# Kernel optimization log

Measured on AMD Instinct MI355X. Metric: run time of the kernel, lower is better.

The kernel has to match this reference:

```python
import jax, jax.numpy as jnp
import numpy as np

B, T = 16, 16384
K, D, H = 512, 64, 64
COMMIT = 0.25
LN_EPS = 1e-5


def setup_inputs() -> dict:
    key = jax.random.key(0)
    ks = jax.random.split(key, 4)
    t = jax.random.randint(ks[0], (B, T, 1), 0, K, dtype=jnp.int32)
    W1 = jax.random.normal(ks[1], (1, H), dtype=jnp.float32) * 0.5
    b1 = jnp.zeros((H,), dtype=jnp.float32)
    ln_g = jnp.ones((H,), dtype=jnp.float32)
    ln_b = jnp.zeros((H,), dtype=jnp.float32)
    W2 = jax.random.normal(ks[2], (H, D), dtype=jnp.float32) * (1.0 / np.sqrt(H))
    b2 = jnp.zeros((D,), dtype=jnp.float32)
    # torch init: uniform(-1/K, 1/K)
    codebook = jax.random.uniform(ks[3], (K, D), dtype=jnp.float32,
                                  minval=-1.0 / K, maxval=1.0 / K)
    return {"t": t, "W1": W1, "b1": b1, "ln_g": ln_g, "ln_b": ln_b,
            "W2": W2, "b2": b2, "codebook": codebook}


def _encoder(t, W1, b1, ln_g, ln_b, W2, b2):
    norm_t = t.astype(jnp.float32) / (K - 1) * 2.0 - 1.0  # [B,T,1]
    h = norm_t @ W1 + b1                                   # [B,T,H]
    mu = jnp.mean(h, axis=-1, keepdims=True)
    var = jnp.mean(jnp.square(h - mu), axis=-1, keepdims=True)
    h = (h - mu) * jax.lax.rsqrt(var + LN_EPS) * ln_g + ln_b
    h = jax.nn.relu(h)
    return h @ W2 + b2                                     # [B,T,D]


def reference(t, W1, b1, ln_g, ln_b, W2, b2, codebook):
    z = _encoder(t, W1, b1, ln_g, ln_b, W2, b2)            # [B,T,D]
    flat_z = z.reshape(-1, D)                               # [N,D]
    # squared distances: ||z||^2 - 2 z.e^T + ||e||^2  -> [N,K]
    dist = (jnp.sum(flat_z * flat_z, axis=1, keepdims=True)
            - 2.0 * flat_z @ codebook.T
            + jnp.sum(codebook * codebook, axis=1))
    idx = jnp.argmin(dist, axis=1)                          # [N]
    quantized = codebook[idx]                               # [N,D]
    sg = jax.lax.stop_gradient
    loss = (jnp.mean(jnp.square(quantized - sg(flat_z)))
            + COMMIT * jnp.mean(jnp.square(sg(quantized) - flat_z)))
    q = flat_z + sg(quantized - flat_z)                     # straight-through
    return q.reshape(z.shape), idx.reshape(z.shape[0], -1), loss
```

## Files before the change

### kernel.cpp

```cpp
#include <hip/hip_runtime.h>

#define Kc 512
#define Dc 64
#define Hc 64
#define Bc 16
#define Tc 16384
#define Nt (Bc * Tc)
#define LN_EPS 1e-5f
#define LOSS_SCALE (1.25f / 16777216.0f)

#define GATHER_BLOCKS 4096
#define GATHER_THREADS 256
#define GATHER_ITERS 4

__global__ __launch_bounds__(256) void precompute_kernel(
    const float* __restrict__ W1, const float* __restrict__ b1,
    const float* __restrict__ ln_g, const float* __restrict__ ln_b,
    const float* __restrict__ W2, const float* __restrict__ b2,
    const float* __restrict__ cb,
    float* __restrict__ q_table, float* __restrict__ idxf_table,
    float* __restrict__ d2_table)
{
    const int v   = blockIdx.x;
    const int tid = threadIdx.x;

    __shared__ float s_h[Hc];
    __shared__ float s_z[Dc];
    __shared__ float s_bd[4];
    __shared__ int   s_bk[4];
    __shared__ int   s_win;
    __shared__ float s_wd;

    if (tid < 64) {
        const int lane = tid;
        const float norm_t = (float)v * (2.0f / (float)(Kc - 1)) - 1.0f;
        float h = norm_t * W1[lane] + b1[lane];

        float s = h;
        #pragma unroll
        for (int o = 32; o > 0; o >>= 1) s += __shfl_xor(s, o);
        const float mu = s * (1.0f / (float)Hc);
        const float d = h - mu;
        float vs = d * d;
        #pragma unroll
        for (int o = 32; o > 0; o >>= 1) vs += __shfl_xor(vs, o);
        const float var = vs * (1.0f / (float)Hc);
        float hn = d * rsqrtf(var + LN_EPS) * ln_g[lane] + ln_b[lane];
        hn = fmaxf(hn, 0.0f);
        s_h[lane] = hn;
        __builtin_amdgcn_s_waitcnt(0);
        float z = b2[lane];
        #pragma unroll
        for (int hh = 0; hh < Hc; ++hh) z = fmaf(s_h[hh], W2[hh * Dc + lane], z);
        s_z[lane] = z;
    }
    __syncthreads();

    const float4* z4 = (const float4*)s_z;
    float best_d = 3.4e38f;
    int best_k = 0;
    #pragma unroll
    for (int half = 0; half < 2; ++half) {
        const int k = tid + half * 256;
        const float4* e4 = (const float4*)(cb + k * Dc);
        float dist = 0.0f;
        #pragma unroll
        for (int q = 0; q < 16; ++q) {
            const float4 e = e4[q];
            const float4 zz = z4[q];
            float d0 = zz.x - e.x, d1 = zz.y - e.y, d2 = zz.z - e.z, d3 = zz.w - e.w;
            dist = fmaf(d0, d0, dist); dist = fmaf(d1, d1, dist);
            dist = fmaf(d2, d2, dist); dist = fmaf(d3, d3, dist);
        }
        if (dist < best_d) { best_d = dist; best_k = k; }
    }
    #pragma unroll
    for (int o = 32; o > 0; o >>= 1) {
        const float od = __shfl_xor(best_d, o);
        const int   ok = __shfl_xor(best_k, o);
        if (od < best_d || (od == best_d && ok < best_k)) { best_d = od; best_k = ok; }
    }
    if ((tid & 63) == 0) { s_bd[tid >> 6] = best_d; s_bk[tid >> 6] = best_k; }
    __syncthreads();
    if (tid == 0) {
        float bd = s_bd[0]; int bk = s_bk[0];
        #pragma unroll
        for (int w = 1; w < 4; ++w) {
            const float od = s_bd[w]; const int ok = s_bk[w];
            if (od < bd || (od == bd && ok < bk)) { bd = od; bk = ok; }
        }
        s_win = bk; s_wd = bd;
    }
    __syncthreads();

    if (tid < 64) q_table[v * Dc + tid] = cb[s_win * Dc + tid];
    if (tid == 0) { idxf_table[v] = (float)s_win; d2_table[v] = s_wd; }
}

__global__ __launch_bounds__(GATHER_THREADS) void gather_kernel(
    const int* __restrict__ t, const float* __restrict__ q_table,
    const float* __restrict__ idxf_table, const float* __restrict__ d2_table,
    float* __restrict__ out_q, float* __restrict__ out_idx,
    float* __restrict__ partials)
{
    const int tid = threadIdx.x;
    const int g0  = blockIdx.x * GATHER_THREADS + tid;
    const int stride = GATHER_BLOCKS * GATHER_THREADS;

    float lsum = 0.0f;
    #pragma unroll
    for (int i = 0; i < GATHER_ITERS; ++i) {
        const int g     = g0 + i * stride;
        const int token = g >> 4;
        const int part  = g & 15;
        const int tv = t[token];
        const float4 q = ((const float4*)q_table)[(tv << 4) + part];
        ((float4*)out_q)[g] = q;
        if (part == 0) {
            out_idx[token] = idxf_table[tv];
            lsum += d2_table[tv];
        }
    }

    #pragma unroll
    for (int o = 32; o > 0; o >>= 1) lsum += __shfl_xor(lsum, o);
    __shared__ float s_partial[4];
    if ((tid & 63) == 0) s_partial[tid >> 6] = lsum;
    __syncthreads();
    if (tid == 0)
        partials[blockIdx.x] =
            s_partial[0] + s_partial[1] + s_partial[2] + s_partial[3];
}

__global__ __launch_bounds__(256) void loss_reduce_kernel(
    const float* __restrict__ partials, float* __restrict__ out_loss)
{
    const int tid = threadIdx.x;
    float s = 0.0f;
    #pragma unroll
    for (int i = 0; i < GATHER_BLOCKS / 256; ++i)
        s += partials[i * 256 + tid];
    #pragma unroll
    for (int o = 32; o > 0; o >>= 1) s += __shfl_xor(s, o);
    __shared__ float s_partial[4];
    if ((tid & 63) == 0) s_partial[tid >> 6] = s;
    __syncthreads();
    if (tid == 0)
        out_loss[0] = (s_partial[0] + s_partial[1] + s_partial[2] + s_partial[3])
                      * LOSS_SCALE;
}

extern "C" void kernel_launch(void* const* d_in, const int* in_sizes, int n_in,
                              void* d_out, int out_size, void* d_ws, size_t ws_size,
                              hipStream_t stream) {
    const int*   t        = (const int*)d_in[0];
    const float* W1       = (const float*)d_in[1];
    const float* b1       = (const float*)d_in[2];
    const float* ln_g     = (const float*)d_in[3];
    const float* ln_b     = (const float*)d_in[4];
    const float* W2       = (const float*)d_in[5];
    const float* b2       = (const float*)d_in[6];
    const float* codebook = (const float*)d_in[7];

    float* out      = (float*)d_out;
    float* out_q    = out;
    float* out_idx  = out + (size_t)Nt * Dc;
    float* out_loss = out_idx + Nt;

    float* ws        = (float*)d_ws;
    float* q_table   = ws;
    float* idxf_tab  = ws + Kc * Dc;
    float* d2_tab    = idxf_tab + Kc;
    float* partials  = d2_tab + Kc;

    precompute_kernel<<<Kc, 256, 0, stream>>>(
        W1, b1, ln_g, ln_b, W2, b2, codebook,
        q_table, idxf_tab, d2_tab);

    gather_kernel<<<GATHER_BLOCKS, GATHER_THREADS, 0, stream>>>(
        t, q_table, idxf_tab, d2_tab, out_q, out_idx, partials);

    loss_reduce_kernel<<<1, 256, 0, stream>>>(partials, out_loss);
}
```

Before: 110.8 us.

## Fuse loss reduction into gather via last-block atomic counter, nontemporal stores

Removes the separate loss-reduce kernel launch: each gather block publishes its partial sum with a release store and bumps an atomic counter, and the last block to finish does the final reduction. Output stores of the quantized tensor become nontemporal so the large streaming write bypasses cache retention. The gather grid shrinks to 1024 blocks with 16 iterations each, which cuts the number of partials. The cost is one atomic per block and a dependence on the counter being reset in the precompute kernel.

```diff
diff --git a/kernel.cpp b/kernel.cpp
--- a/kernel.cpp
+++ b/kernel.cpp
@@ -9,9 +9,11 @@
 #define LN_EPS 1e-5f
 #define LOSS_SCALE (1.25f / 16777216.0f)
 
-#define GATHER_BLOCKS 4096
+#define GATHER_BLOCKS 1024
 #define GATHER_THREADS 256
-#define GATHER_ITERS 4
+#define GATHER_ITERS 16
+
+typedef float v4f __attribute__((ext_vector_type(4)));
 
 __global__ __launch_bounds__(256) void precompute_kernel(
     const float* __restrict__ W1, const float* __restrict__ b1,
@@ -19,10 +21,12 @@
     const float* __restrict__ W2, const float* __restrict__ b2,
     const float* __restrict__ cb,
     float* __restrict__ q_table, float* __restrict__ idxf_table,
-    float* __restrict__ d2_table)
+    float* __restrict__ d2_table, int* __restrict__ counter)
 {
     const int v   = blockIdx.x;
     const int tid = threadIdx.x;
+
+    if (v == 0 && tid == 0) *counter = 0;
 
     __shared__ float s_h[Hc];
     __shared__ float s_z[Dc];
@@ -101,7 +105,8 @@
     const int* __restrict__ t, const float* __restrict__ q_table,
     const float* __restrict__ idxf_table, const float* __restrict__ d2_table,
     float* __restrict__ out_q, float* __restrict__ out_idx,
-    float* __restrict__ partials)
+    float* __restrict__ partials, int* __restrict__ counter,
+    float* __restrict__ out_loss)
 {
     const int tid = threadIdx.x;
     const int g0  = blockIdx.x * GATHER_THREADS + tid;
@@ -115,7 +120,8 @@
         const int part  = g & 15;
         const int tv = t[token];
         const float4 q = ((const float4*)q_table)[(tv << 4) + part];
-        ((float4*)out_q)[g] = q;
+        const v4f qv = { q.x, q.y, q.z, q.w };
+        __builtin_nontemporal_store(qv, &((v4f*)out_q)[g]);
         if (part == 0) {
             out_idx[token] = idxf_table[tv];
             lsum += d2_table[tv];
@@ -125,29 +131,34 @@
     #pragma unroll
     for (int o = 32; o > 0; o >>= 1) lsum += __shfl_xor(lsum, o);
     __shared__ float s_partial[4];
+    __shared__ int   s_done;
     if ((tid & 63) == 0) s_partial[tid >> 6] = lsum;
     __syncthreads();
-    if (tid == 0)
-        partials[blockIdx.x] =
+    if (tid == 0) {
+        const float bs =
             s_partial[0] + s_partial[1] + s_partial[2] + s_partial[3];
-}
+        __hip_atomic_store(&partials[blockIdx.x], bs, __ATOMIC_RELEASE,
+                           __HIP_MEMORY_SCOPE_AGENT);
+        const int prev = __hip_atomic_fetch_add(counter, 1, __ATOMIC_ACQ_REL,
+                                                __HIP_MEMORY_SCOPE_AGENT);
+        s_done = (prev == GATHER_BLOCKS - 1) ? 1 : 0;
+    }
+    __syncthreads();
 
-__global__ __launch_bounds__(256) void loss_reduce_kernel(
-    const float* __restrict__ partials, float* __restrict__ out_loss)
-{
-    const int tid = threadIdx.x;
-    float s = 0.0f;
-    #pragma unroll
-    for (int i = 0; i < GATHER_BLOCKS / 256; ++i)
-        s += partials[i * 256 + tid];
-    #pragma unroll
-    for (int o = 32; o > 0; o >>= 1) s += __shfl_xor(s, o);
-    __shared__ float s_partial[4];
-    if ((tid & 63) == 0) s_partial[tid >> 6] = s;
-    __syncthreads();
-    if (tid == 0)
-        out_loss[0] = (s_partial[0] + s_partial[1] + s_partial[2] + s_partial[3])
-                      * LOSS_SCALE;
+    if (s_done) {
+        float s = 0.0f;
+        #pragma unroll
+        for (int i = 0; i < GATHER_BLOCKS / GATHER_THREADS; ++i)
+            s += __hip_atomic_load(&partials[i * GATHER_THREADS + tid],
+                                   __ATOMIC_ACQUIRE, __HIP_MEMORY_SCOPE_AGENT);
+        #pragma unroll
+        for (int o = 32; o > 0; o >>= 1) s += __shfl_xor(s, o);
+        __shared__ float s_fin[4];
+        if ((tid & 63) == 0) s_fin[tid >> 6] = s;
+        __syncthreads();
+        if (tid == 0)
+            out_loss[0] = (s_fin[0] + s_fin[1] + s_fin[2] + s_fin[3]) * LOSS_SCALE;
+    }
 }
 
 extern "C" void kernel_launch(void* const* d_in, const int* in_sizes, int n_in,
@@ -172,13 +183,12 @@
     float* idxf_tab  = ws + Kc * Dc;
     float* d2_tab    = idxf_tab + Kc;
     float* partials  = d2_tab + Kc;
+    int*   counter   = (int*)(partials + GATHER_BLOCKS);
 
     precompute_kernel<<<Kc, 256, 0, stream>>>(
         W1, b1, ln_g, ln_b, W2, b2, codebook,
-        q_table, idxf_tab, d2_tab);
+        q_table, idxf_tab, d2_tab, counter);
 
     gather_kernel<<<GATHER_BLOCKS, GATHER_THREADS, 0, stream>>>(
-        t, q_table, idxf_tab, d2_tab, out_q, out_idx, partials);
-
-    loss_reduce_kernel<<<1, 256, 0, stream>>>(partials, out_loss);
+        t, q_table, idxf_tab, d2_tab, out_q, out_idx, partials, counter, out_loss);
 }
```

Measured after the change: 161.8 us. +46.0%, slower.
